# Optimization experiments

Measured on AMD Instinct MI355X. Metric: run time of the kernel, lower is better.

The kernel has to match this reference:

```python
import jax, jax.numpy as jnp
import numpy as np

DIM = 1024        # model dim
HEADS = 1         # num_heads (fc1 in_features==1 forces this)
HDIM = DIM // HEADS
INNER = 16        # dim_inner
B, L = 2, 4096
ROPE_BASE = 32.0


def _apply_rope(x, pos, base):
    # x: [b, l, h, d]; standard rotate-half RoPE
    d = x.shape[-1]
    inv_freq = base ** (-jnp.arange(0, d, 2, dtype=jnp.float32) / d)   # [d/2]
    ang = pos[:, None].astype(jnp.float32) * inv_freq                  # [l, d/2]
    emb = jnp.concatenate([ang, ang], axis=-1)                         # [l, d]
    cos = jnp.cos(emb)[None, :, None, :].astype(x.dtype)
    sin = jnp.sin(emb)[None, :, None, :].astype(x.dtype)
    x1, x2 = x[..., : d // 2], x[..., d // 2:]
    rot = jnp.concatenate([-x2, x1], axis=-1)
    return x * cos + rot * sin


def setup_inputs() -> dict:
    key = jax.random.key(0)
    ks = jax.random.split(key, 7)
    hidden_states = jax.random.normal(ks[0], (B, L, DIM), dtype=jnp.float32)
    Wq = jax.random.normal(ks[1], (DIM, DIM), dtype=jnp.float32) * 0.02
    Wk = jax.random.normal(ks[2], (DIM, DIM), dtype=jnp.float32) * 0.02
    fc1_w = jax.random.normal(ks[3], (INNER, 1), dtype=jnp.float32) * 0.1
    fc1_b = jax.random.normal(ks[4], (INNER,), dtype=jnp.float32) * 0.1
    fc2_w = jax.random.normal(ks[5], (DIM, INNER), dtype=jnp.float32) * 0.1
    fc2_b = jax.random.normal(ks[6], (DIM,), dtype=jnp.float32) * 0.1
    return {"hidden_states": hidden_states, "Wq": Wq, "Wk": Wk,
            "fc1_w": fc1_w, "fc1_b": fc1_b, "fc2_w": fc2_w, "fc2_b": fc2_b}


def reference(hidden_states, Wq, Wk, fc1_w, fc1_b, fc2_w, fc2_b):
    b, l, _ = hidden_states.shape
    # projections, cast to bf16 as in the torch module
    q = (hidden_states @ Wq.T).reshape(b, l, HEADS, HDIM).astype(jnp.bfloat16)
    k = (hidden_states @ Wk.T).reshape(b, l, HEADS, HDIM).astype(jnp.bfloat16)
    pos = jnp.arange(l)
    q = _apply_rope(q, pos, ROPE_BASE)
    k = _apply_rope(k, pos, ROPE_BASE)
    # causal exp(QK) with NO softmax normalization; accumulate in fp32
    scores = jnp.einsum('bqhd,bkhd->bhqk',
                        q.astype(jnp.float32), k.astype(jnp.float32)) / (HDIM ** 0.5)
    causal = jnp.tril(jnp.ones((l, l), dtype=bool))                    # [l, l]
    exp_qk = jnp.where(causal[None, None], jnp.exp(scores), 0.0)       # [b, h, l, l]
    o = jnp.swapaxes(exp_qk.sum(axis=-1), 1, 2)                        # [b, l, h]
    # small MLP: h(=1) -> INNER -> DIM
    o = jax.nn.relu(o @ fc1_w.T + fc1_b)
    return o @ fc2_w.T + fc2_b                                         # [b, l, DIM]
```

## Files before the change

kernel.cpp:

```cpp
#include <hip/hip_runtime.h>
#include <hip/hip_bf16.h>

typedef __bf16 bf16_t;
typedef __bf16 bf16x4 __attribute__((ext_vector_type(4)));
typedef __bf16 bf16x8 __attribute__((ext_vector_type(8)));
typedef float f32x4 __attribute__((ext_vector_type(4)));

#define B_   2
#define L_   4096
#define DIM_ 1024
#define M_   (B_ * L_)
#define NTASK2_ 272

__device__ __forceinline__ void ld_g2l_16(const bf16_t* g, bf16_t* l) {
  __builtin_amdgcn_global_load_lds(
      (__attribute__((address_space(1))) void*)g,
      (__attribute__((address_space(3))) void*)l, 16, 0, 0);
}

__global__ void cvt_all(const float* __restrict__ hs, const float* __restrict__ wq,
                        const float* __restrict__ wk, bf16_t* __restrict__ hs_b,
                        bf16_t* __restrict__ wq_b, bf16_t* __restrict__ wk_b) {
  const int N_HS = M_ * DIM_ / 4, N_W = DIM_ * DIM_ / 4;
  int i = blockIdx.x * blockDim.x + threadIdx.x;
  const float* s; bf16_t* d; int idx;
  if (i < N_HS)            { s = hs; d = hs_b; idx = i; }
  else if (i < N_HS + N_W) { s = wq; d = wq_b; idx = i - N_HS; }
  else                     { s = wk; d = wk_b; idx = i - N_HS - N_W; }
  float4 v = ((const float4*)s)[idx];
  bf16x4 o = { (bf16_t)v.x, (bf16_t)v.y, (bf16_t)v.z, (bf16_t)v.w };
  ((bf16x4*)d)[idx] = o;
}

#define SLICE_SEGS_ 24
#define BUFSZ_ (SLICE_SEGS_ * 512)

__device__ __forceinline__ void core_256x128_pipe(const bf16_t* __restrict__ A,
                                                  const bf16_t* __restrict__ B,
                                                  bf16_t* sm, bool active,
                                                  f32x4 (&acc)[4][4]) {
  const int tid  = threadIdx.x;
  const int wave = tid >> 6, lane = tid & 63;
  const int wm = wave >> 1, wn = wave & 1;
  const int quad = lane >> 4, l16 = lane & 15;
  const int srow = lane >> 2;
  const int scol = (((lane & 3) ^ ((lane >> 3) & 3)) * 8);
  const int rsw  = ((l16 >> 1) & 3) * 8;
  const int loff = l16 * 32 + ((quad * 8) ^ rsw);

  const bf16_t* gA0 = A + (size_t)(wave * 16 + srow) * DIM_ + scol;
  const bf16_t* gA1 = A + (size_t)((wave + 8) * 16 + srow) * DIM_ + scol;
  const bf16_t* gB  = B + (size_t)(wave * 16 + srow) * DIM_ + scol;

  bf16_t* p0 = sm;
  bf16_t* p1 = sm + BUFSZ_;
  bf16_t* p2 = sm + 2 * BUFSZ_;

  ld_g2l_16(gA0,      p0 + wave * 512);
  ld_g2l_16(gA1,      p0 + (wave + 8) * 512);
  ld_g2l_16(gB,       p0 + (16 + wave) * 512);
  ld_g2l_16(gA0 + 32, p1 + wave * 512);
  ld_g2l_16(gA1 + 32, p1 + (wave + 8) * 512);
  ld_g2l_16(gB  + 32, p1 + (16 + wave) * 512);
  gA0 += 64; gA1 += 64; gB += 64;
  asm volatile("s_waitcnt vmcnt(3)" ::: "memory");
  __builtin_amdgcn_s_barrier();

  for (int s = 0; s < 32; ++s) {
    bf16x8 aF[4], bF[4];
    if (active) {
#pragma unroll
      for (int rf = 0; rf < 4; ++rf)
        aF[rf] = *(const bf16x8*)(p0 + (wm * 4 + rf) * 512 + loff);
#pragma unroll
      for (int cf = 0; cf < 4; ++cf)
        bF[cf] = *(const bf16x8*)(p0 + (16 + wn * 4 + cf) * 512 + loff);
    }
    if (s < 30) {
      ld_g2l_16(gA0, p2 + wave * 512);
      ld_g2l_16(gA1, p2 + (wave + 8) * 512);
      ld_g2l_16(gB,  p2 + (16 + wave) * 512);
      gA0 += 32; gA1 += 32; gB += 32;
    }
    __builtin_amdgcn_s_barrier();
    asm volatile("s_waitcnt lgkmcnt(0)" ::: "memory");
    __builtin_amdgcn_sched_barrier(0);
    if (active) {
      __builtin_amdgcn_s_setprio(1);
#pragma unroll
      for (int rf = 0; rf < 4; ++rf)
#pragma unroll
        for (int cf = 0; cf < 4; ++cf)
          acc[rf][cf] = __builtin_amdgcn_mfma_f32_16x16x32_bf16(
              aF[rf], bF[cf], acc[rf][cf], 0, 0, 0);
      __builtin_amdgcn_s_setprio(0);
    }
    if (s < 30)       asm volatile("s_waitcnt vmcnt(3)" ::: "memory");
    else if (s == 30) asm volatile("s_waitcnt vmcnt(0)" ::: "memory");
    __builtin_amdgcn_s_barrier();
    bf16_t* t0 = p0; p0 = p1; p1 = p2; p2 = t0;
  }
}

__global__ __launch_bounds__(512, 2)
void proj_gemm(const bf16_t* __restrict__ A, const bf16_t* __restrict__ Wqb,
               const bf16_t* __restrict__ Wkb, bf16_t* __restrict__ Cq,
               bf16_t* __restrict__ Ck) {
  __shared__ __attribute__((aligned(16))) bf16_t sm[3 * BUFSZ_];
  const bf16_t* Bm = (blockIdx.z == 0) ? Wqb : Wkb;
  bf16_t* Cm = (blockIdx.z == 0) ? Cq : Ck;
  const int m0 = blockIdx.y * 256, n0 = blockIdx.x * 128;

  f32x4 acc[4][4] = {};
  core_256x128_pipe(A + (size_t)m0 * DIM_, Bm + (size_t)n0 * DIM_, sm, true, acc);

  const int tid = threadIdx.x, wave = tid >> 6, lane = tid & 63;
  const int wm = wave >> 1, wn = wave & 1;
  const int quad = lane >> 4, l16 = lane & 15;
#pragma unroll
  for (int rf = 0; rf < 4; ++rf)
#pragma unroll
    for (int cf = 0; cf < 4; ++cf)
#pragma unroll
      for (int r = 0; r < 4; ++r) {
        int m = m0 + wm * 64 + rf * 16 + quad * 4 + r;
        int n = n0 + wn * 64 + cf * 16 + l16;
        Cm[(size_t)m * DIM_ + n] = (bf16_t)acc[rf][cf][r];
      }
}

__global__ void rope_kernel(bf16_t* __restrict__ q, bf16_t* __restrict__ k) {
  bf16_t* x = blockIdx.y ? k : q;
  int row = blockIdx.x * 2 + (threadIdx.x >> 7);
  int j0  = (threadIdx.x & 127) * 4;
  int pos = row & (L_ - 1);
  bf16_t* p = x + (size_t)row * DIM_;
  bf16x4 v1 = *(const bf16x4*)(p + j0);
  bf16x4 v2 = *(const bf16x4*)(p + j0 + 512);
  bf16x4 o1, o2;
#pragma unroll
  for (int u = 0; u < 4; ++u) {
    int j = j0 + u;
    float ang = (float)pos * exp2f((float)j * (-5.0f / 512.0f));
    float c = cosf(ang), s = sinf(ang);
    float cb = (float)(bf16_t)c, sb = (float)(bf16_t)s;
    float x1 = (float)v1[u], x2 = (float)v2[u];
    o1[u] = (bf16_t)(x1 * cb - x2 * sb);
    o2[u] = (bf16_t)(x2 * cb + x1 * sb);
  }
  *(bf16x4*)(p + j0) = o1;
  *(bf16x4*)(p + j0 + 512) = o2;
}

__global__ __launch_bounds__(512, 2)
void attn_rowsum(const bf16_t* __restrict__ Q, const bf16_t* __restrict__ Kc,
                 float* __restrict__ o) {
  __shared__ __attribute__((aligned(16))) bf16_t sm[3 * BUFSZ_];
  int t = blockIdx.x;
  int b = t / NTASK2_;
  t -= b * NTASK2_;
  int mi = (int)((sqrtf(4.0f * (float)t + 1.0f) - 1.0f) * 0.5f);
  while ((mi + 1) * (mi + 2) <= t) ++mi;
  while (mi * (mi + 1) > t) --mi;
  int nt = t - mi * (mi + 1);

  const int tid = threadIdx.x, wave = tid >> 6, lane = tid & 63;
  const int wm = wave >> 1, wn = wave & 1;
  const int quad = lane >> 4, l16 = lane & 15;

  const bf16_t* A  = Q  + (size_t)b * L_ * DIM_ + (size_t)mi * 256 * DIM_;
  const bf16_t* Bp = Kc + (size_t)b * L_ * DIM_ + (size_t)nt * 128 * DIM_;

  bool active = (mi * 256 + wm * 64 + 63) >= nt * 128;

  f32x4 acc[4][4] = {};
  core_256x128_pipe(A, Bp, sm, active, acc);

  if (active) {
    const bool masked = (nt >= 2 * mi);
#pragma unroll
    for (int rf = 0; rf < 4; ++rf) {
#pragma unroll
      for (int r = 0; r < 4; ++r) {
        int grow = mi * 256 + wm * 64 + rf * 16 + quad * 4 + r;
        float sum = 0.0f;
#pragma unroll
        for (int cf = 0; cf < 4; ++cf) {
          int gcol = nt * 128 + wn * 64 + cf * 16 + l16;
          float e = __expf(acc[rf][cf][r] * 0.03125f);
          if (!masked || gcol <= grow) sum += e;
        }
        sum += __shfl_xor(sum, 1);
        sum += __shfl_xor(sum, 2);
        sum += __shfl_xor(sum, 4);
        sum += __shfl_xor(sum, 8);
        if (l16 == 0)
          atomicAdd(&o[b * L_ + grow], sum);
      }
    }
  }
}

__global__ __launch_bounds__(256)
void mlp_out_kernel(const float* __restrict__ o, const float* __restrict__ fc1_w,
                    const float* __restrict__ fc1_b, const float* __restrict__ fc2_w,
                    const float* __restrict__ fc2_b, float* __restrict__ out) {
  const int R = 16;
  int row0 = blockIdx.x * R;
  int tid = threadIdx.x;
  __shared__ float h[R][16];
  {
    int rl = tid >> 4, i = tid & 15;
    float s = o[row0 + rl];
    h[rl][i] = fmaxf(fc1_w[i] * s + fc1_b[i], 0.0f);
  }
  __syncthreads();
  int d = tid * 4;
  float w[4][16];
#pragma unroll
  for (int c = 0; c < 4; ++c)
#pragma unroll
    for (int i = 0; i < 16; ++i) w[c][i] = fc2_w[(d + c) * 16 + i];
  float4 bb = *(const float4*)(fc2_b + d);
  for (int rl = 0; rl < R; ++rl) {
    float4 v = bb;
#pragma unroll
    for (int i = 0; i < 16; ++i) {
      float hv = h[rl][i];
      v.x += w[0][i] * hv; v.y += w[1][i] * hv;
      v.z += w[2][i] * hv; v.w += w[3][i] * hv;
    }
    *(float4*)(out + (size_t)(row0 + rl) * DIM_ + d) = v;
  }
}

extern "C" void kernel_launch(void* const* d_in, const int* in_sizes, int n_in,
                              void* d_out, int out_size, void* d_ws, size_t ws_size,
                              hipStream_t stream) {
  const float* hs    = (const float*)d_in[0];
  const float* Wq    = (const float*)d_in[1];
  const float* Wk    = (const float*)d_in[2];
  const float* fc1_w = (const float*)d_in[3];
  const float* fc1_b = (const float*)d_in[4];
  const float* fc2_w = (const float*)d_in[5];
  const float* fc2_b = (const float*)d_in[6];
  float* out = (float*)d_out;

  char* ws = (char*)d_ws;
  bf16_t* hs_bf = (bf16_t*)ws; ws += (size_t)M_ * DIM_ * 2;
  bf16_t* wq_bf = (bf16_t*)ws; ws += (size_t)DIM_ * DIM_ * 2;
  bf16_t* wk_bf = (bf16_t*)ws; ws += (size_t)DIM_ * DIM_ * 2;
  bf16_t* q_bf  = (bf16_t*)ws; ws += (size_t)M_ * DIM_ * 2;
  bf16_t* k_bf  = (bf16_t*)ws; ws += (size_t)M_ * DIM_ * 2;
  float*  o     = (float*)ws;

  const int n4 = (M_ * DIM_ + 2 * DIM_ * DIM_) / 4;
  cvt_all<<<n4 / 256, 256, 0, stream>>>(hs, Wq, Wk, hs_bf, wq_bf, wk_bf);

  dim3 gg(DIM_ / 128, M_ / 256, 2);
  proj_gemm<<<gg, 512, 0, stream>>>(hs_bf, wq_bf, wk_bf, q_bf, k_bf);

  dim3 gr(M_ / 2, 2);
  rope_kernel<<<gr, 256, 0, stream>>>(q_bf, k_bf);

  hipMemsetAsync(o, 0, M_ * sizeof(float), stream);
  attn_rowsum<<<B_ * NTASK2_, 512, 0, stream>>>(q_bf, k_bf, o);

  mlp_out_kernel<<<M_ / 16, 256, 0, stream>>>(o, fc1_w, fc1_b, fc2_w, fc2_b, out);
}
```

Measured before the change: 229.5 us.

## Fuse RoPE into projection GEMM epilogue and fold memset into conversion

```diff
diff --git a/kernel.cpp b/kernel.cpp
--- a/kernel.cpp
+++ b/kernel.cpp
@@ -20,25 +20,28 @@
 
 __global__ void cvt_all(const float* __restrict__ hs, const float* __restrict__ wq,
                         const float* __restrict__ wk, bf16_t* __restrict__ hs_b,
-                        bf16_t* __restrict__ wq_b, bf16_t* __restrict__ wk_b) {
+                        bf16_t* __restrict__ wq_b, bf16_t* __restrict__ wk_b,
+                        float* __restrict__ o) {
   const int N_HS = M_ * DIM_ / 4, N_W = DIM_ * DIM_ / 4;
   int i = blockIdx.x * blockDim.x + threadIdx.x;
+  if (i < M_ / 4) ((float4*)o)[i] = float4{0.f, 0.f, 0.f, 0.f};
   const float* s; bf16_t* d; int idx;
   if (i < N_HS)            { s = hs; d = hs_b; idx = i; }
   else if (i < N_HS + N_W) { s = wq; d = wq_b; idx = i - N_HS; }
   else                     { s = wk; d = wk_b; idx = i - N_HS - N_W; }
   float4 v = ((const float4*)s)[idx];
-  bf16x4 o = { (bf16_t)v.x, (bf16_t)v.y, (bf16_t)v.z, (bf16_t)v.w };
-  ((bf16x4*)d)[idx] = o;
-}
-
-#define SLICE_SEGS_ 24
-#define BUFSZ_ (SLICE_SEGS_ * 512)
-
-__device__ __forceinline__ void core_256x128_pipe(const bf16_t* __restrict__ A,
-                                                  const bf16_t* __restrict__ B,
-                                                  bf16_t* sm, bool active,
-                                                  f32x4 (&acc)[4][4]) {
+  bf16x4 ov = { (bf16_t)v.x, (bf16_t)v.y, (bf16_t)v.z, (bf16_t)v.w };
+  ((bf16x4*)d)[idx] = ov;
+}
+
+template <int BSEGS>
+__device__ __forceinline__ void core256(const bf16_t* __restrict__ A,
+                                        const bf16_t* __restrict__ B0,
+                                        const bf16_t* __restrict__ B1,
+                                        bf16_t* sm, bool active,
+                                        f32x4 (&acc)[4][BSEGS / 2]) {
+  constexpr int SEGS = 16 + BSEGS;
+  constexpr int BUF  = SEGS * 512;
   const int tid  = threadIdx.x;
   const int wave = tid >> 6, lane = tid & 63;
   const int wm = wave >> 1, wn = wave & 1;
@@ -50,55 +53,63 @@
 
   const bf16_t* gA0 = A + (size_t)(wave * 16 + srow) * DIM_ + scol;
   const bf16_t* gA1 = A + (size_t)((wave + 8) * 16 + srow) * DIM_ + scol;
-  const bf16_t* gB  = B + (size_t)(wave * 16 + srow) * DIM_ + scol;
-
-  bf16_t* p0 = sm;
-  bf16_t* p1 = sm + BUFSZ_;
-  bf16_t* p2 = sm + 2 * BUFSZ_;
-
-  ld_g2l_16(gA0,      p0 + wave * 512);
-  ld_g2l_16(gA1,      p0 + (wave + 8) * 512);
-  ld_g2l_16(gB,       p0 + (16 + wave) * 512);
-  ld_g2l_16(gA0 + 32, p1 + wave * 512);
-  ld_g2l_16(gA1 + 32, p1 + (wave + 8) * 512);
-  ld_g2l_16(gB  + 32, p1 + (16 + wave) * 512);
-  gA0 += 64; gA1 += 64; gB += 64;
-  asm volatile("s_waitcnt vmcnt(3)" ::: "memory");
+  const bf16_t* gB0 = B0 + (size_t)(wave * 16 + srow) * DIM_ + scol;
+  const bf16_t* gB1 = gB0;
+  if constexpr (BSEGS == 16) gB1 = B1 + (size_t)(wave * 16 + srow) * DIM_ + scol;
+
+  bf16_t* pb0 = sm;
+  bf16_t* pb1 = sm + BUF;
+
+  auto stage = [&](int kk, bf16_t* buf) {
+    ld_g2l_16(gA0 + kk, buf + wave * 512);
+    ld_g2l_16(gA1 + kk, buf + (wave + 8) * 512);
+    ld_g2l_16(gB0 + kk, buf + (16 + wave) * 512);
+    if constexpr (BSEGS == 16) ld_g2l_16(gB1 + kk, buf + (24 + wave) * 512);
+  };
+
+  stage(0, pb0);
+  stage(32, pb1);
+  if constexpr (BSEGS == 16) asm volatile("s_waitcnt vmcnt(4)" ::: "memory");
+  else                       asm volatile("s_waitcnt vmcnt(3)" ::: "memory");
   __builtin_amdgcn_s_barrier();
+  __builtin_amdgcn_sched_barrier(0);
 
   for (int s = 0; s < 32; ++s) {
-    bf16x8 aF[4], bF[4];
+    bf16_t* cur = (s & 1) ? pb1 : pb0;
+    bf16x8 aF[4], bF[BSEGS / 2];
     if (active) {
 #pragma unroll
       for (int rf = 0; rf < 4; ++rf)
-        aF[rf] = *(const bf16x8*)(p0 + (wm * 4 + rf) * 512 + loff);
-#pragma unroll
-      for (int cf = 0; cf < 4; ++cf)
-        bF[cf] = *(const bf16x8*)(p0 + (16 + wn * 4 + cf) * 512 + loff);
-    }
-    if (s < 30) {
-      ld_g2l_16(gA0, p2 + wave * 512);
-      ld_g2l_16(gA1, p2 + (wave + 8) * 512);
-      ld_g2l_16(gB,  p2 + (16 + wave) * 512);
-      gA0 += 32; gA1 += 32; gB += 32;
-    }
-    __builtin_amdgcn_s_barrier();
+        aF[rf] = *(const bf16x8*)(cur + (wm * 4 + rf) * 512 + loff);
+#pragma unroll
+      for (int cf = 0; cf < BSEGS / 2; ++cf) {
+        int k = (cf & 3) + wn * 4 + (cf >> 2) * 8;
+        bF[cf] = *(const bf16x8*)(cur + (16 + k) * 512 + loff);
+      }
+    }
     asm volatile("s_waitcnt lgkmcnt(0)" ::: "memory");
     __builtin_amdgcn_sched_barrier(0);
+    __builtin_amdgcn_s_barrier();
+    __builtin_amdgcn_sched_barrier(0);
+    if (s + 2 < 32) stage((s + 2) * 32, cur);
     if (active) {
       __builtin_amdgcn_s_setprio(1);
 #pragma unroll
       for (int rf = 0; rf < 4; ++rf)
 #pragma unroll
-        for (int cf = 0; cf < 4; ++cf)
+        for (int cf = 0; cf < BSEGS / 2; ++cf)
           acc[rf][cf] = __builtin_amdgcn_mfma_f32_16x16x32_bf16(
               aF[rf], bF[cf], acc[rf][cf], 0, 0, 0);
       __builtin_amdgcn_s_setprio(0);
     }
-    if (s < 30)       asm volatile("s_waitcnt vmcnt(3)" ::: "memory");
-    else if (s == 30) asm volatile("s_waitcnt vmcnt(0)" ::: "memory");
+    if (s < 30) {
+      if constexpr (BSEGS == 16) asm volatile("s_waitcnt vmcnt(4)" ::: "memory");
+      else                       asm volatile("s_waitcnt vmcnt(3)" ::: "memory");
+    } else if (s == 30) {
+      asm volatile("s_waitcnt vmcnt(0)" ::: "memory");
+    }
     __builtin_amdgcn_s_barrier();
-    bf16_t* t0 = p0; p0 = p1; p1 = p2; p2 = t0;
+    __builtin_amdgcn_sched_barrier(0);
   }
 }
 
@@ -106,59 +117,55 @@
 void proj_gemm(const bf16_t* __restrict__ A, const bf16_t* __restrict__ Wqb,
                const bf16_t* __restrict__ Wkb, bf16_t* __restrict__ Cq,
                bf16_t* __restrict__ Ck) {
-  __shared__ __attribute__((aligned(16))) bf16_t sm[3 * BUFSZ_];
-  const bf16_t* Bm = (blockIdx.z == 0) ? Wqb : Wkb;
-  bf16_t* Cm = (blockIdx.z == 0) ? Cq : Ck;
-  const int m0 = blockIdx.y * 256, n0 = blockIdx.x * 128;
-
-  f32x4 acc[4][4] = {};
-  core_256x128_pipe(A + (size_t)m0 * DIM_, Bm + (size_t)n0 * DIM_, sm, true, acc);
+  __shared__ __attribute__((aligned(16))) bf16_t sm[2 * 32 * 512];
+  int logical = ((blockIdx.x & 7) << 5) | (blockIdx.x >> 3);
+  int zn = logical >> 5;
+  int z = zn >> 2, n0 = (zn & 3) * 128;
+  int m0 = (logical & 31) * 256;
+  const bf16_t* Wb = z ? Wkb : Wqb;
+  bf16_t* Cm = z ? Ck : Cq;
+
+  f32x4 acc[4][8] = {};
+  core256<16>(A + (size_t)m0 * DIM_, Wb + (size_t)n0 * DIM_,
+              Wb + (size_t)(n0 + 512) * DIM_, sm, true, acc);
 
   const int tid = threadIdx.x, wave = tid >> 6, lane = tid & 63;
   const int wm = wave >> 1, wn = wave & 1;
   const int quad = lane >> 4, l16 = lane & 15;
+
+  float inv[4];
+#pragma unroll
+  for (int cf = 0; cf < 4; ++cf) {
+    int j = n0 + wn * 64 + cf * 16 + l16;
+    inv[cf] = exp2f((float)j * (-5.0f / 512.0f));
+  }
 #pragma unroll
   for (int rf = 0; rf < 4; ++rf)
 #pragma unroll
-    for (int cf = 0; cf < 4; ++cf)
-#pragma unroll
-      for (int r = 0; r < 4; ++r) {
-        int m = m0 + wm * 64 + rf * 16 + quad * 4 + r;
-        int n = n0 + wn * 64 + cf * 16 + l16;
-        Cm[(size_t)m * DIM_ + n] = (bf16_t)acc[rf][cf][r];
+    for (int r = 0; r < 4; ++r) {
+      int m = m0 + wm * 64 + rf * 16 + quad * 4 + r;
+      float posf = (float)(m & (L_ - 1));
+#pragma unroll
+      for (int cf = 0; cf < 4; ++cf) {
+        int j = n0 + wn * 64 + cf * 16 + l16;
+        float ang = posf * inv[cf];
+        float c = cosf(ang), s = sinf(ang);
+        float cb = (float)(bf16_t)c, sb = (float)(bf16_t)s;
+        float x1 = (float)(bf16_t)acc[rf][cf][r];
+        float x2 = (float)(bf16_t)acc[rf][cf + 4][r];
+        Cm[(size_t)m * DIM_ + j]       = (bf16_t)(x1 * cb - x2 * sb);
+        Cm[(size_t)m * DIM_ + j + 512] = (bf16_t)(x2 * cb + x1 * sb);
       }
-}
-
-__global__ void rope_kernel(bf16_t* __restrict__ q, bf16_t* __restrict__ k) {
-  bf16_t* x = blockIdx.y ? k : q;
-  int row = blockIdx.x * 2 + (threadIdx.x >> 7);
-  int j0  = (threadIdx.x & 127) * 4;
-  int pos = row & (L_ - 1);
-  bf16_t* p = x + (size_t)row * DIM_;
-  bf16x4 v1 = *(const bf16x4*)(p + j0);
-  bf16x4 v2 = *(const bf16x4*)(p + j0 + 512);
-  bf16x4 o1, o2;
-#pragma unroll
-  for (int u = 0; u < 4; ++u) {
-    int j = j0 + u;
-    float ang = (float)pos * exp2f((float)j * (-5.0f / 512.0f));
-    float c = cosf(ang), s = sinf(ang);
-    float cb = (float)(bf16_t)c, sb = (float)(bf16_t)s;
-    float x1 = (float)v1[u], x2 = (float)v2[u];
-    o1[u] = (bf16_t)(x1 * cb - x2 * sb);
-    o2[u] = (bf16_t)(x2 * cb + x1 * sb);
-  }
-  *(bf16x4*)(p + j0) = o1;
-  *(bf16x4*)(p + j0 + 512) = o2;
-}
-
-__global__ __launch_bounds__(512, 2)
+    }
+}
+
+__global__ __launch_bounds__(512, 4)
 void attn_rowsum(const bf16_t* __restrict__ Q, const bf16_t* __restrict__ Kc,
                  float* __restrict__ o) {
-  __shared__ __attribute__((aligned(16))) bf16_t sm[3 * BUFSZ_];
-  int t = blockIdx.x;
-  int b = t / NTASK2_;
-  t -= b * NTASK2_;
+  __shared__ __attribute__((aligned(16))) bf16_t sm[2 * 24 * 512];
+  int logical = (blockIdx.x & 7) * 68 + (blockIdx.x >> 3);
+  int b = logical / NTASK2_;
+  int t = logical - b * NTASK2_;
   int mi = (int)((sqrtf(4.0f * (float)t + 1.0f) - 1.0f) * 0.5f);
   while ((mi + 1) * (mi + 2) <= t) ++mi;
   while (mi * (mi + 1) > t) --mi;
@@ -174,7 +181,7 @@
   bool active = (mi * 256 + wm * 64 + 63) >= nt * 128;
 
   f32x4 acc[4][4] = {};
-  core_256x128_pipe(A, Bp, sm, active, acc);
+  core256<8>(A, Bp, nullptr, sm, active, acc);
 
   if (active) {
     const bool masked = (nt >= 2 * mi);
@@ -255,16 +262,11 @@
   float*  o     = (float*)ws;
 
   const int n4 = (M_ * DIM_ + 2 * DIM_ * DIM_) / 4;
-  cvt_all<<<n4 / 256, 256, 0, stream>>>(hs, Wq, Wk, hs_bf, wq_bf, wk_bf);
-
-  dim3 gg(DIM_ / 128, M_ / 256, 2);
-  proj_gemm<<<gg, 512, 0, stream>>>(hs_bf, wq_bf, wk_bf, q_bf, k_bf);
-
-  dim3 gr(M_ / 2, 2);
-  rope_kernel<<<gr, 256, 0, stream>>>(q_bf, k_bf);
-
-  hipMemsetAsync(o, 0, M_ * sizeof(float), stream);
-  attn_rowsum<<<B_ * NTASK2_, 512, 0, stream>>>(q_bf, k_bf, o);
+  cvt_all<<<n4 / 256, 256, 0, stream>>>(hs, Wq, Wk, hs_bf, wq_bf, wk_bf, o);
+
+  proj_gemm<<<256, 512, 0, stream>>>(hs_bf, wq_bf, wk_bf, q_bf, k_bf);
+
+  attn_rowsum<<<544, 512, 0, stream>>>(q_bf, k_bf, o);
 
   mlp_out_kernel<<<M_ / 16, 256, 0, stream>>>(o, fc1_w, fc1_b, fc2_w, fc2_b, out);
 }
```

Result: slower. 261.5 us (+13.9%).
